# Optimization experiments

Hardware: AMD Instinct MI355X
Metric: run time of the kernel (lower is better)

The kernel has to match this reference:

```python
import jax, jax.numpy as jnp
import numpy as np

N_SITES = 500000   # active voxels
K = 27             # 3^3 filter offsets
R = 250000         # rule-book pairs per offset
C_IN = 16
C_OUT = 16


def setup_inputs() -> dict:
    key = jax.random.key(0)
    k1, k2, k3, k4 = jax.random.split(key, 4)
    std = (2.0 / C_IN / K) ** 0.5
    features = jax.random.normal(k1, (N_SITES, C_IN), dtype=jnp.float32)
    weight = jax.random.normal(k2, (K, C_IN, C_OUT), dtype=jnp.float32) * std
    bias = jnp.zeros((C_OUT,), dtype=jnp.float32)
    rules_in = jax.random.randint(k3, (K, R), 0, N_SITES, dtype=jnp.int32)
    rules_out = jax.random.randint(k4, (K, R), 0, N_SITES, dtype=jnp.int32)
    return {"features": features, "weight": weight, "bias": bias,
            "rules_in": rules_in, "rules_out": rules_out}


def reference(features, weight, bias, rules_in, rules_out):
    # Submanifold conv as rule-book gather -> per-offset GEMM -> scatter-add.
    # features: [N, Cin], weight: [K, Cin, Cout], rules_*: [K, R]
    gathered = features[rules_in]                         # [K, R, Cin]
    contrib = jnp.einsum('krc,kco->kro', gathered, weight)  # [K, R, Cout]
    n = features.shape[0]
    out = jnp.broadcast_to(bias, (n, weight.shape[2])).astype(features.dtype)
    out = out.at[rules_out.reshape(-1)].add(
        contrib.reshape(-1, weight.shape[2]))             # scatter-add into active sites
    return out
```

## Files before the change

kernel.cpp:

```cpp
#include <hip/hip_runtime.h>

#define NSITES 500000
#define KOFF   27
#define RPAIR  250000
#define KR     (KOFF * RPAIR)
#define CIN    16
#define COUT   16
#define NBUCK  1954
#define NBLK   256
#define CHUNK  ((KR + NBLK - 1) / NBLK)
#define NSLICE 31
#define ASTRIDE 17
#define IDXCAP 4096

#define OFF_PT     1000448
#define OFF_TTOT   2000896
#define OFF_CSTART 2008712
#define OFF_ENT    2016544
#define OFF_FBF16  29016544
#define NEED_BF16  45016544
#define NEED_F32   29016544

__global__ __launch_bounds__(256) void convert_bf16_kernel(
    const float* __restrict__ f, uint4* __restrict__ fb)
{
    const int r = blockIdx.x * 256 + threadIdx.x;
    if (r >= NSITES) return;
    const uint4* src = (const uint4*)(f + (size_t)r * CIN);
    const uint4 a = src[0], b = src[1], c = src[2], d = src[3];
#define BF(x) (((x) + 0x7FFFu + (((x) >> 16) & 1u)) >> 16)
    uint4 o0, o1;
    o0.x = BF(a.x) | (BF(a.y) << 16);
    o0.y = BF(a.z) | (BF(a.w) << 16);
    o0.z = BF(b.x) | (BF(b.y) << 16);
    o0.w = BF(b.z) | (BF(b.w) << 16);
    o1.x = BF(c.x) | (BF(c.y) << 16);
    o1.y = BF(c.z) | (BF(c.w) << 16);
    o1.z = BF(d.x) | (BF(d.y) << 16);
    o1.w = BF(d.z) | (BF(d.w) << 16);
#undef BF
    fb[(size_t)r * 2]     = o0;
    fb[(size_t)r * 2 + 1] = o1;
}

__global__ __launch_bounds__(256) void passA_kernel(
    const int* __restrict__ rules_out, unsigned short* __restrict__ countsT)
{
    __shared__ unsigned cnt[NBUCK];
    for (int i = threadIdx.x; i < NBUCK; i += 256) cnt[i] = 0;
    __syncthreads();
    const int base = blockIdx.x * CHUNK;
    const int end  = (base + CHUNK < KR) ? base + CHUNK : KR;
    for (int p = base + threadIdx.x; p < end; p += 256)
        atomicAdd(&cnt[rules_out[p] >> 8], 1u);
    __syncthreads();
    unsigned short* row = countsT + (size_t)blockIdx.x * NBUCK;
    for (int i = threadIdx.x; i < NBUCK; i += 256)
        row[i] = (unsigned short)cnt[i];
}

__global__ __launch_bounds__(256) void scanK1_kernel(
    const unsigned short* __restrict__ countsT,
    unsigned short* __restrict__ PT, int* __restrict__ Ttot)
{
    const int c = blockIdx.x * 256 + threadIdx.x;
    if (c >= NBUCK) return;
    unsigned run = 0;
    for (int g = 0; g < NBLK; ++g) {
        PT[(size_t)g * NBUCK + c] = (unsigned short)run;
        run += countsT[(size_t)g * NBUCK + c];
    }
    Ttot[c] = (int)run;
}

__global__ __launch_bounds__(1024) void scanK2_kernel(
    const int* __restrict__ Ttot, int* __restrict__ cstart)
{
    __shared__ int s[1024];
    __shared__ int base_s;
    const int t = threadIdx.x;
    if (t == 0) base_s = 0;
    __syncthreads();
    for (int chunk = 0; chunk < (NBUCK + 1023) / 1024; ++chunk) {
        const int i = chunk * 1024 + t;
        const int v = (i < NBUCK) ? Ttot[i] : 0;
        s[t] = v;
        __syncthreads();
        for (int off = 1; off < 1024; off <<= 1) {
            int u = (t >= off) ? s[t - off] : 0;
            __syncthreads();
            s[t] += u;
            __syncthreads();
        }
        if (i < NBUCK) cstart[i] = base_s + s[t] - v;
        __syncthreads();
        if (t == 1023) base_s += s[1023];
        __syncthreads();
    }
    if (t == 0) cstart[NBUCK] = KR;
}

__global__ __launch_bounds__(256) void passB_kernel(
    const int* __restrict__ rules_in, const int* __restrict__ rules_out,
    const int* __restrict__ cstart, const unsigned short* __restrict__ PT,
    unsigned* __restrict__ entries)
{
    __shared__ unsigned cur[NBUCK];
    for (int i = threadIdx.x; i < NBUCK; i += 256) cur[i] = 0;
    __syncthreads();
    const int base = blockIdx.x * CHUNK;
    const int end  = (base + CHUNK < KR) ? base + CHUNK : KR;
    const unsigned short* pt = PT + (size_t)blockIdx.x * NBUCK;
    for (int p = base + threadIdx.x; p < end; p += 256) {
        const int o  = rules_out[p];
        const int in = rules_in[p];
        const int b  = o >> 8;
        const int k  = p / RPAIR;
        const unsigned rank = atomicAdd(&cur[b], 1u);
        const int pos = cstart[b] + (int)pt[b] + (int)rank;
        entries[pos] = (unsigned)in | ((unsigned)k << 19) |
                       ((unsigned)(o & 255) << 24);
    }
}

__device__ __forceinline__ void fma4(float4& a, float s, const float4 w) {
    a.x = fmaf(s, w.x, a.x);
    a.y = fmaf(s, w.y, a.y);
    a.z = fmaf(s, w.z, a.z);
    a.w = fmaf(s, w.w, a.w);
}

template <int BF16>
__device__ __forceinline__ void process_entry(
    unsigned v, const uint4* __restrict__ fb, const float* __restrict__ feat,
    const float* __restrict__ weight, float* acc)
{
    const int in = v & 0x7FFFF;
    const int k  = (v >> 19) & 31;
    const int ol = (int)(v >> 24);
    float f[16];
    if (BF16) {
        const uint4 pa = fb[(size_t)in * 2];
        const uint4 pb = fb[(size_t)in * 2 + 1];
        f[0]  = __uint_as_float(pa.x << 16); f[1]  = __uint_as_float(pa.x & 0xFFFF0000u);
        f[2]  = __uint_as_float(pa.y << 16); f[3]  = __uint_as_float(pa.y & 0xFFFF0000u);
        f[4]  = __uint_as_float(pa.z << 16); f[5]  = __uint_as_float(pa.z & 0xFFFF0000u);
        f[6]  = __uint_as_float(pa.w << 16); f[7]  = __uint_as_float(pa.w & 0xFFFF0000u);
        f[8]  = __uint_as_float(pb.x << 16); f[9]  = __uint_as_float(pb.x & 0xFFFF0000u);
        f[10] = __uint_as_float(pb.y << 16); f[11] = __uint_as_float(pb.y & 0xFFFF0000u);
        f[12] = __uint_as_float(pb.z << 16); f[13] = __uint_as_float(pb.z & 0xFFFF0000u);
        f[14] = __uint_as_float(pb.w << 16); f[15] = __uint_as_float(pb.w & 0xFFFF0000u);
    } else {
        const float4* f4 = (const float4*)(feat + (size_t)in * CIN);
        const float4 q0 = f4[0], q1 = f4[1], q2 = f4[2], q3 = f4[3];
        f[0]=q0.x; f[1]=q0.y; f[2]=q0.z; f[3]=q0.w;
        f[4]=q1.x; f[5]=q1.y; f[6]=q1.z; f[7]=q1.w;
        f[8]=q2.x; f[9]=q2.y; f[10]=q2.z; f[11]=q2.w;
        f[12]=q3.x; f[13]=q3.y; f[14]=q3.z; f[15]=q3.w;
    }
    const float4* w4 = (const float4*)(weight + k * (CIN * COUT));
    float4 a0 = make_float4(0.f, 0.f, 0.f, 0.f);
    float4 a1 = a0, a2 = a0, a3 = a0;
#define CSTEP(c)                           \
    {                                      \
        const float s_ = f[c];             \
        fma4(a0, s_, w4[(c) * 4 + 0]);     \
        fma4(a1, s_, w4[(c) * 4 + 1]);     \
        fma4(a2, s_, w4[(c) * 4 + 2]);     \
        fma4(a3, s_, w4[(c) * 4 + 3]);     \
    }
    CSTEP(0)  CSTEP(1)  CSTEP(2)  CSTEP(3)
    CSTEP(4)  CSTEP(5)  CSTEP(6)  CSTEP(7)
    CSTEP(8)  CSTEP(9)  CSTEP(10) CSTEP(11)
    CSTEP(12) CSTEP(13) CSTEP(14) CSTEP(15)
#undef CSTEP
    float* ar = acc + ol * ASTRIDE;
    atomicAdd(ar +  0, a0.x); atomicAdd(ar +  1, a0.y);
    atomicAdd(ar +  2, a0.z); atomicAdd(ar +  3, a0.w);
    atomicAdd(ar +  4, a1.x); atomicAdd(ar +  5, a1.y);
    atomicAdd(ar +  6, a1.z); atomicAdd(ar +  7, a1.w);
    atomicAdd(ar +  8, a2.x); atomicAdd(ar +  9, a2.y);
    atomicAdd(ar + 10, a2.z); atomicAdd(ar + 11, a2.w);
    atomicAdd(ar + 12, a3.x); atomicAdd(ar + 13, a3.y);
    atomicAdd(ar + 14, a3.z); atomicAdd(ar + 15, a3.w);
}

template <int BF16>
__global__ __launch_bounds__(256) void bucket_gemm_kernel(
    const uint4* __restrict__ fb,
    const float* __restrict__ feat,
    const float* __restrict__ weight,
    const float* __restrict__ bias,
    const int*   __restrict__ cstart,
    const unsigned* __restrict__ entries,
    float*       __restrict__ out)
{
    __shared__ float acc[256 * ASTRIDE];
    __shared__ unsigned short idx[IDXCAP];
    __shared__ unsigned scnt[NSLICE];
    __shared__ unsigned sdone;
    const int b   = blockIdx.x;
    const int tid = threadIdx.x;

    for (int i = tid; i < 256 * ASTRIDE; i += 256) acc[i] = 0.f;
    if (tid < NSLICE) scnt[tid] = 0;
    if (tid == 0) sdone = 0;
    __syncthreads();

    const int s0 = cstart[b];
    const int e0 = cstart[b + 1];
    const int n  = e0 - s0;
    const int nl = (n < IDXCAP) ? n : IDXCAP;

    for (int i = tid; i < nl; i += 256) {
        const unsigned v = entries[s0 + i];
        atomicAdd(&scnt[(v & 0x7FFFFu) >> 14], 1u);
    }
    __syncthreads();
    if (tid == 0) {
        unsigned run = 0;
        for (int s = 0; s < NSLICE; ++s) {
            const unsigned c = scnt[s];
            scnt[s] = run;
            run += c;
        }
    }
    __syncthreads();
    for (int i = tid; i < nl; i += 256) {
        const unsigned v = entries[s0 + i];
        const unsigned slot = atomicAdd(&scnt[(v & 0x7FFFFu) >> 14], 1u);
        idx[slot] = (unsigned short)i;
    }
    __syncthreads();
    for (int j = tid; j < nl; j += 256) {
        const unsigned v = entries[s0 + (int)idx[j]];
        process_entry<BF16>(v, fb, feat, weight, acc);
    }
    for (int i = nl + tid; i < n; i += 256) {
        process_entry<BF16>(entries[s0 + i], fb, feat, weight, acc);
    }
    __syncthreads();

    const int row = b * 256 + tid;
    if (row >= NSITES) return;
    const float* a = acc + tid * ASTRIDE;
    float4 o0, o1, o2, o3;
    o0.x = a[ 0] + bias[ 0]; o0.y = a[ 1] + bias[ 1];
    o0.z = a[ 2] + bias[ 2]; o0.w = a[ 3] + bias[ 3];
    o1.x = a[ 4] + bias[ 4]; o1.y = a[ 5] + bias[ 5];
    o1.z = a[ 6] + bias[ 6]; o1.w = a[ 7] + bias[ 7];
    o2.x = a[ 8] + bias[ 8]; o2.y = a[ 9] + bias[ 9];
    o2.z = a[10] + bias[10]; o2.w = a[11] + bias[11];
    o3.x = a[12] + bias[12]; o3.y = a[13] + bias[13];
    o3.z = a[14] + bias[14]; o3.w = a[15] + bias[15];
    float4* op = (float4*)(out + (size_t)row * COUT);
    op[0] = o0; op[1] = o1; op[2] = o2; op[3] = o3;
}

extern "C" void kernel_launch(void* const* d_in, const int* in_sizes, int n_in,
                              void* d_out, int out_size, void* d_ws, size_t ws_size,
                              hipStream_t stream)
{
    const float* features  = (const float*)d_in[0];
    const float* weight    = (const float*)d_in[1];
    const float* bias      = (const float*)d_in[2];
    const int*   rules_in  = (const int*)d_in[3];
    const int*   rules_out = (const int*)d_in[4];
    float*       out       = (float*)d_out;

    char* wsb = (char*)d_ws;
    unsigned short* countsT = (unsigned short*)wsb;
    unsigned short* PT      = (unsigned short*)(wsb + OFF_PT);
    int*            Ttot    = (int*)(wsb + OFF_TTOT);
    int*            cstart  = (int*)(wsb + OFF_CSTART);
    unsigned*       entries = (unsigned*)(wsb + OFF_ENT);
    uint4*          fbf16   = (uint4*)(wsb + OFF_FBF16);

    const bool use_bf16 = (ws_size >= (size_t)NEED_BF16);

    if (use_bf16) {
        convert_bf16_kernel<<<(NSITES + 255) / 256, 256, 0, stream>>>(
            features, fbf16);
    }

    passA_kernel<<<NBLK, 256, 0, stream>>>(rules_out, countsT);
    scanK1_kernel<<<(NBUCK + 255) / 256, 256, 0, stream>>>(countsT, PT, Ttot);
    scanK2_kernel<<<1, 1024, 0, stream>>>(Ttot, cstart);
    passB_kernel<<<NBLK, 256, 0, stream>>>(rules_in, rules_out, cstart, PT,
                                           entries);

    if (use_bf16) {
        bucket_gemm_kernel<1><<<NBUCK, 256, 0, stream>>>(
            fbf16, features, weight, bias, cstart, entries, out);
    } else {
        bucket_gemm_kernel<0><<<NBUCK, 256, 0, stream>>>(
            fbf16, features, weight, bias, cstart, entries, out);
    }
}
```

Measured before the change: 927.0 us.

## Split output buckets by input-range slices with fp16 partials and a reduce pass

The rule-book sort now keys on the output bucket plus an 8-way input-row slice. This lets each GEMM block gather from a narrow range of the bf16 feature table, replacing the per-block in-LDS slice sort. When the workspace is large enough, each segment writes fp16 partial sums to global memory and a separate reduce kernel adds the slices and the bias. In exchange the count/prefix arrays grow 8x, an extra partials round-trip and kernel are added, and the fp16 partials lose precision. Rule loads are also made nontemporal.

```diff
diff --git a/kernel.cpp b/kernel.cpp
--- a/kernel.cpp
+++ b/kernel.cpp
@@ -1,4 +1,5 @@
 #include <hip/hip_runtime.h>
+#include <hip/hip_fp16.h>
 
 #define NSITES 500000
 #define KOFF   27
@@ -7,19 +8,24 @@
 #define CIN    16
 #define COUT   16
 #define NBUCK  1954
+#define NSLC   8
+#define NSEG   (NBUCK * NSLC)
 #define NBLK   256
 #define CHUNK  ((KR + NBLK - 1) / NBLK)
-#define NSLICE 31
 #define ASTRIDE 17
-#define IDXCAP 4096
-
-#define OFF_PT     1000448
-#define OFF_TTOT   2000896
-#define OFF_CSTART 2008712
-#define OFF_ENT    2016544
-#define OFF_FBF16  29016544
-#define NEED_BF16  45016544
-#define NEED_F32   29016544
+#define PROWS  (NBUCK * 256)
+
+typedef unsigned uvec4 __attribute__((ext_vector_type(4)));
+
+#define OFF_CNT   0ull
+#define OFF_PT    8003584ull
+#define OFF_TTOT  16007168ull
+#define OFF_CST   16069696ull
+#define OFF_ENT   16132288ull
+#define OFF_FB    43132288ull
+#define OFF_PART  59132288ull
+#define NEED_FULL 187189632ull
+#define NEED_MID  59132288ull
 
 __global__ __launch_bounds__(256) void convert_bf16_kernel(
     const float* __restrict__ f, uint4* __restrict__ fb)
@@ -44,18 +50,22 @@
 }
 
 __global__ __launch_bounds__(256) void passA_kernel(
-    const int* __restrict__ rules_out, unsigned short* __restrict__ countsT)
-{
-    __shared__ unsigned cnt[NBUCK];
-    for (int i = threadIdx.x; i < NBUCK; i += 256) cnt[i] = 0;
+    const int* __restrict__ rules_in, const int* __restrict__ rules_out,
+    unsigned short* __restrict__ countsT)
+{
+    __shared__ unsigned cnt[NSEG];
+    for (int i = threadIdx.x; i < NSEG; i += 256) cnt[i] = 0;
     __syncthreads();
     const int base = blockIdx.x * CHUNK;
     const int end  = (base + CHUNK < KR) ? base + CHUNK : KR;
-    for (int p = base + threadIdx.x; p < end; p += 256)
-        atomicAdd(&cnt[rules_out[p] >> 8], 1u);
-    __syncthreads();
-    unsigned short* row = countsT + (size_t)blockIdx.x * NBUCK;
-    for (int i = threadIdx.x; i < NBUCK; i += 256)
+    for (int p = base + threadIdx.x; p < end; p += 256) {
+        const int o  = __builtin_nontemporal_load(rules_out + p);
+        const int in = __builtin_nontemporal_load(rules_in + p);
+        atomicAdd(&cnt[((o >> 8) << 3) | (in >> 16)], 1u);
+    }
+    __syncthreads();
+    unsigned short* row = countsT + (size_t)blockIdx.x * NSEG;
+    for (int i = threadIdx.x; i < NSEG; i += 256)
         row[i] = (unsigned short)cnt[i];
 }
 
@@ -64,11 +74,11 @@
     unsigned short* __restrict__ PT, int* __restrict__ Ttot)
 {
     const int c = blockIdx.x * 256 + threadIdx.x;
-    if (c >= NBUCK) return;
+    if (c >= NSEG) return;
     unsigned run = 0;
     for (int g = 0; g < NBLK; ++g) {
-        PT[(size_t)g * NBUCK + c] = (unsigned short)run;
-        run += countsT[(size_t)g * NBUCK + c];
+        PT[(size_t)g * NSEG + c] = (unsigned short)run;
+        run += countsT[(size_t)g * NSEG + c];
     }
     Ttot[c] = (int)run;
 }
@@ -81,9 +91,9 @@
     const int t = threadIdx.x;
     if (t == 0) base_s = 0;
     __syncthreads();
-    for (int chunk = 0; chunk < (NBUCK + 1023) / 1024; ++chunk) {
+    for (int chunk = 0; chunk < (NSEG + 1023) / 1024; ++chunk) {
         const int i = chunk * 1024 + t;
-        const int v = (i < NBUCK) ? Ttot[i] : 0;
+        const int v = (i < NSEG) ? Ttot[i] : 0;
         s[t] = v;
         __syncthreads();
         for (int off = 1; off < 1024; off <<= 1) {
@@ -92,12 +102,12 @@
             s[t] += u;
             __syncthreads();
         }
-        if (i < NBUCK) cstart[i] = base_s + s[t] - v;
+        if (i < NSEG) cstart[i] = base_s + s[t] - v;
         __syncthreads();
         if (t == 1023) base_s += s[1023];
         __syncthreads();
     }
-    if (t == 0) cstart[NBUCK] = KR;
+    if (t == 0) cstart[NSEG] = KR;
 }
 
 __global__ __launch_bounds__(256) void passB_kernel(
@@ -105,19 +115,19 @@
     const int* __restrict__ cstart, const unsigned short* __restrict__ PT,
     unsigned* __restrict__ entries)
 {
-    __shared__ unsigned cur[NBUCK];
-    for (int i = threadIdx.x; i < NBUCK; i += 256) cur[i] = 0;
+    __shared__ unsigned cur[NSEG];
+    for (int i = threadIdx.x; i < NSEG; i += 256) cur[i] = 0;
     __syncthreads();
     const int base = blockIdx.x * CHUNK;
     const int end  = (base + CHUNK < KR) ? base + CHUNK : KR;
-    const unsigned short* pt = PT + (size_t)blockIdx.x * NBUCK;
+    const unsigned short* pt = PT + (size_t)blockIdx.x * NSEG;
     for (int p = base + threadIdx.x; p < end; p += 256) {
-        const int o  = rules_out[p];
-        const int in = rules_in[p];
-        const int b  = o >> 8;
-        const int k  = p / RPAIR;
-        const unsigned rank = atomicAdd(&cur[b], 1u);
-        const int pos = cstart[b] + (int)pt[b] + (int)rank;
+        const int o   = __builtin_nontemporal_load(rules_out + p);
+        const int in  = __builtin_nontemporal_load(rules_in + p);
+        const int seg = ((o >> 8) << 3) | (in >> 16);
+        const int k   = p / RPAIR;
+        const unsigned rank = atomicAdd(&cur[seg], 1u);
+        const int pos = cstart[seg] + (int)pt[seg] + (int)rank;
         entries[pos] = (unsigned)in | ((unsigned)k << 19) |
                        ((unsigned)(o & 255) << 24);
     }
@@ -185,8 +195,79 @@
     atomicAdd(ar + 14, a3.z); atomicAdd(ar + 15, a3.w);
 }
 
+__global__ __launch_bounds__(256) void gemm_full_kernel(
+    const uint4* __restrict__ fb,
+    const float* __restrict__ weight,
+    const int*   __restrict__ cstart,
+    const unsigned* __restrict__ entries,
+    char*        __restrict__ partials)
+{
+    __shared__ float acc[256 * ASTRIDE];
+    const int seg = blockIdx.x;
+    const int b   = seg >> 3;
+    const int x   = seg & 7;
+    const int tid = threadIdx.x;
+
+    for (int i = tid; i < 256 * ASTRIDE; i += 256) acc[i] = 0.f;
+    __syncthreads();
+
+    const int s = cstart[seg];
+    const int e = cstart[seg + 1];
+    for (int i = s + tid; i < e; i += 256) {
+        const unsigned v = __builtin_nontemporal_load(entries + i);
+        process_entry<1>(v, fb, (const float*)nullptr, weight, acc);
+    }
+    __syncthreads();
+
+    const float* a = acc + tid * ASTRIDE;
+    unsigned hw[8];
+#pragma unroll
+    for (int i = 0; i < 8; ++i) {
+        __half2 h = __floats2half2_rn(a[2 * i], a[2 * i + 1]);
+        hw[i] = *(unsigned*)&h;
+    }
+    uvec4 s0 = {hw[0], hw[1], hw[2], hw[3]};
+    uvec4 s1 = {hw[4], hw[5], hw[6], hw[7]};
+    uvec4* dst = (uvec4*)(partials +
+                 ((size_t)x * PROWS + (size_t)b * 256 + tid) * 32);
+    __builtin_nontemporal_store(s0, dst);
+    __builtin_nontemporal_store(s1, dst + 1);
+}
+
+__global__ __launch_bounds__(256) void reduce_kernel(
+    const char* __restrict__ partials, const float* __restrict__ bias,
+    float* __restrict__ out)
+{
+    const int row = blockIdx.x * 256 + threadIdx.x;
+    if (row >= NSITES) return;
+    float s[16];
+#pragma unroll
+    for (int c = 0; c < 16; ++c) s[c] = bias[c];
+#pragma unroll
+    for (int x = 0; x < NSLC; ++x) {
+        const uvec4* p = (const uvec4*)(partials +
+                         ((size_t)x * PROWS + row) * 32);
+        const uvec4 u0 = __builtin_nontemporal_load(p);
+        const uvec4 u1 = __builtin_nontemporal_load(p + 1);
+        const unsigned w[8] = {u0.x, u0.y, u0.z, u0.w, u1.x, u1.y, u1.z, u1.w};
+#pragma unroll
+        for (int i = 0; i < 8; ++i) {
+            __half2 h = *(const __half2*)&w[i];
+            const float2 f = __half22float2(h);
+            s[2 * i]     += f.x;
+            s[2 * i + 1] += f.y;
+        }
+    }
+    float4 o0 = make_float4(s[0], s[1], s[2], s[3]);
+    float4 o1 = make_float4(s[4], s[5], s[6], s[7]);
+    float4 o2 = make_float4(s[8], s[9], s[10], s[11]);
+    float4 o3 = make_float4(s[12], s[13], s[14], s[15]);
+    float4* op = (float4*)(out + (size_t)row * COUT);
+    op[0] = o0; op[1] = o1; op[2] = o2; op[3] = o3;
+}
+
 template <int BF16>
-__global__ __launch_bounds__(256) void bucket_gemm_kernel(
+__global__ __launch_bounds__(256) void gemm_fb_kernel(
     const uint4* __restrict__ fb,
     const float* __restrict__ feat,
     const float* __restrict__ weight,
@@ -196,51 +277,15 @@
     float*       __restrict__ out)
 {
     __shared__ float acc[256 * ASTRIDE];
-    __shared__ unsigned short idx[IDXCAP];
-    __shared__ unsigned scnt[NSLICE];
-    __shared__ unsigned sdone;
     const int b   = blockIdx.x;
     const int tid = threadIdx.x;
-
     for (int i = tid; i < 256 * ASTRIDE; i += 256) acc[i] = 0.f;
-    if (tid < NSLICE) scnt[tid] = 0;
-    if (tid == 0) sdone = 0;
-    __syncthreads();
-
-    const int s0 = cstart[b];
-    const int e0 = cstart[b + 1];
-    const int n  = e0 - s0;
-    const int nl = (n < IDXCAP) ? n : IDXCAP;
-
-    for (int i = tid; i < nl; i += 256) {
-        const unsigned v = entries[s0 + i];
-        atomicAdd(&scnt[(v & 0x7FFFFu) >> 14], 1u);
-    }
-    __syncthreads();
-    if (tid == 0) {
-        unsigned run = 0;
-        for (int s = 0; s < NSLICE; ++s) {
-            const unsigned c = scnt[s];
-            scnt[s] = run;
-            run += c;
-        }
-    }
-    __syncthreads();
-    for (int i = tid; i < nl; i += 256) {
-        const unsigned v = entries[s0 + i];
-        const unsigned slot = atomicAdd(&scnt[(v & 0x7FFFFu) >> 14], 1u);
-        idx[slot] = (unsigned short)i;
-    }
-    __syncthreads();
-    for (int j = tid; j < nl; j += 256) {
-        const unsigned v = entries[s0 + (int)idx[j]];
-        process_entry<BF16>(v, fb, feat, weight, acc);
-    }
-    for (int i = nl + tid; i < n; i += 256) {
-        process_entry<BF16>(entries[s0 + i], fb, feat, weight, acc);
-    }
-    __syncthreads();
-
+    __syncthreads();
+    const int s = cstart[b * NSLC];
+    const int e = cstart[b * NSLC + NSLC];
+    for (int i = s + tid; i < e; i += 256)
+        process_entry<BF16>(entries[i], fb, feat, weight, acc);
+    __syncthreads();
     const int row = b * 256 + tid;
     if (row >= NSITES) return;
     const float* a = acc + tid * ASTRIDE;
@@ -269,31 +314,38 @@
     float*       out       = (float*)d_out;
 
     char* wsb = (char*)d_ws;
-    unsigned short* countsT = (unsigned short*)wsb;
+    unsigned short* countsT = (unsigned short*)(wsb + OFF_CNT);
     unsigned short* PT      = (unsigned short*)(wsb + OFF_PT);
     int*            Ttot    = (int*)(wsb + OFF_TTOT);
-    int*            cstart  = (int*)(wsb + OFF_CSTART);
+    int*            cstart  = (int*)(wsb + OFF_CST);
     unsigned*       entries = (unsigned*)(wsb + OFF_ENT);
-    uint4*          fbf16   = (uint4*)(wsb + OFF_FBF16);
-
-    const bool use_bf16 = (ws_size >= (size_t)NEED_BF16);
-
-    if (use_bf16) {
+    uint4*          fbf16   = (uint4*)(wsb + OFF_FB);
+    char*           partials= wsb + OFF_PART;
+
+    const int tier = (ws_size >= NEED_FULL) ? 2
+                   : (ws_size >= NEED_MID)  ? 1 : 0;
+
+    if (tier >= 1) {
         convert_bf16_kernel<<<(NSITES + 255) / 256, 256, 0, stream>>>(
             features, fbf16);
     }
 
-    passA_kernel<<<NBLK, 256, 0, stream>>>(rules_out, countsT);
-    scanK1_kernel<<<(NBUCK + 255) / 256, 256, 0, stream>>>(countsT, PT, Ttot);
+    passA_kernel<<<NBLK, 256, 0, stream>>>(rules_in, rules_out, countsT);
+    scanK1_kernel<<<(NSEG + 255) / 256, 256, 0, stream>>>(countsT, PT, Ttot);
     scanK2_kernel<<<1, 1024, 0, stream>>>(Ttot, cstart);
     passB_kernel<<<NBLK, 256, 0, stream>>>(rules_in, rules_out, cstart, PT,
                                            entries);
 
-    if (use_bf16) {
-        bucket_gemm_kernel<1><<<NBUCK, 256, 0, stream>>>(
+    if (tier == 2) {
+        gemm_full_kernel<<<NSEG, 256, 0, stream>>>(
+            fbf16, weight, cstart, entries, partials);
+        reduce_kernel<<<(NSITES + 255) / 256, 256, 0, stream>>>(
+            partials, bias, out);
+    } else if (tier == 1) {
+        gemm_fb_kernel<1><<<NBUCK, 256, 0, stream>>>(
             fbf16, features, weight, bias, cstart, entries, out);
     } else {
-        bucket_gemm_kernel<0><<<NBUCK, 256, 0, stream>>>(
+        gemm_fb_kernel<0><<<NBUCK, 256, 0, stream>>>(
             fbf16, features, weight, bias, cstart, entries, out);
     }
 }
```

Measured after the change: 1.093 ms. 1.18x slower.
